# Kernel optimization log

Measured on AMD Instinct MI355X. Metric: run time of the kernel, lower is better.

The kernel has to match this reference:

```python
import jax, jax.numpy as jnp
import numpy as np

WS = 7           # window_size
DIM_HEAD = 32    # qk head dim
NUM_HEAD = 8     # dim_in // dim_head = 256 // 32
DIM_EXP = 1024   # dim_in * exp_ratio
WIN_NUM = 16     # (28 // 7) ** 2
EPS = 1e-5


def _rel_pos_index():
    # same construction as torch buffer; returns [49*49] int index into (2*WS-1)^2 table
    coords = np.stack(np.meshgrid(np.arange(WS), np.arange(WS), indexing='ij'))  # [2,WS,WS]
    cf = coords.reshape(2, -1)                                                   # [2,49]
    rel = cf[:, :, None] - cf[:, None, :]                                        # [2,49,49]
    rel = rel.transpose(1, 2, 0)
    rel[:, :, 0] += WS - 1
    rel[:, :, 1] += WS - 1
    rel[:, :, 0] *= 2 * WS - 1
    return jnp.asarray(rel.sum(-1).reshape(-1), dtype=jnp.int32)                 # [2401]


def _ln_channel(x, w, b):
    # LayerNorm over channel dim (axis=1) of [b,c,h,w], per the 'ln_1d' norm
    mu = jnp.mean(x, axis=1, keepdims=True)
    var = jnp.var(x, axis=1, keepdims=True)
    xn = (x - mu) * jax.lax.rsqrt(var + EPS)
    return xn * w[None, :, None, None] + b[None, :, None, None]


def setup_inputs() -> dict:
    key = jax.random.key(0)
    ks = jax.random.split(key, 12)
    C = 256
    x = jax.random.normal(ks[0], (64, C, 28, 28), dtype=jnp.float32)
    return {
        'x': x,
        'pre_w': jnp.ones((C,), jnp.float32),
        'pre_b': jnp.zeros((C,), jnp.float32),
        'qk_w': jax.random.normal(ks[1], (2 * C, C), jnp.float32) * 0.02,
        'qk_b': jnp.zeros((2 * C,), jnp.float32),
        'v_w': jax.random.normal(ks[2], (DIM_EXP, C), jnp.float32) * 0.02,
        'v_b': jnp.zeros((DIM_EXP,), jnp.float32),
        'post_w': jnp.ones((DIM_EXP // 2,), jnp.float32),
        'post_b': jnp.zeros((DIM_EXP // 2,), jnp.float32),
        'proj_w': jax.random.normal(ks[3], (C, DIM_EXP), jnp.float32) * 0.02,
        'proj_b': jnp.zeros((C,), jnp.float32),
        'rpb_table': jax.random.normal(ks[4], (WIN_NUM, (2 * WS - 1) ** 2, NUM_HEAD), jnp.float32) * 0.02,
    }


def reference(x, pre_w, pre_b, qk_w, qk_b, v_w, v_b, post_w, post_b, proj_w, proj_b, rpb_table):
    B, C, H, W = x.shape
    n1, n2 = H // WS, W // WS
    shortcut = x
    # b c (h1 n1) (w1 n2) -> (b n1 n2) c h1 w1
    xw = x.reshape(B, C, WS, n1, WS, n2).transpose(0, 3, 5, 1, 2, 4).reshape(B * n1 * n2, C, WS, WS)
    b = B * n1 * n2
    xw = _ln_channel(xw, pre_w, pre_b)
    # 1x1 conv QK -> split into q,k per head: channels ordered (qk, heads, dim_head)
    qk = jnp.einsum('oc,bchw->bohw', qk_w, xw) + qk_b[None, :, None, None]
    qk = qk.reshape(b, 2, NUM_HEAD, DIM_HEAD, WS * WS).transpose(1, 0, 2, 4, 3)  # [2,b,h,49,dh]
    q, k = qk[0], qk[1]
    # 1x1 conv V -> attn half + idle half
    v = jnp.einsum('oc,bchw->bohw', v_w, xw) + v_b[None, :, None, None]
    v_attn, v_idle = jnp.split(v, 2, axis=1)                                     # each [b,512,7,7]
    dhv = (DIM_EXP // 2) // NUM_HEAD
    va = v_attn.reshape(b, NUM_HEAD, dhv, WS * WS).transpose(0, 1, 3, 2)         # [b,h,49,dhv]
    # relative position bias (gathered fresh each forward, one table per window)
    idx = _rel_pos_index()
    bias = rpb_table[:, idx, :]                                                  # [wn,2401,nh]
    bias = bias.reshape(WIN_NUM, WS * WS, WS * WS, NUM_HEAD).transpose(0, 3, 1, 2)
    bias = jnp.broadcast_to(bias[None], (B, WIN_NUM, NUM_HEAD, WS * WS, WS * WS)).reshape(b, NUM_HEAD, WS * WS, WS * WS)
    # SDPA (scale = 1/sqrt(q head dim), additive float mask)
    scale = DIM_HEAD ** -0.5
    logits = jnp.einsum('bhqd,bhkd->bhqk', q, k) * scale + bias
    attn = jax.nn.softmax(logits, axis=-1)
    out = jnp.einsum('bhqk,bhkd->bhqd', attn, va)                                # [b,h,49,dhv]
    out = out.transpose(0, 1, 3, 2).reshape(b, DIM_EXP // 2, WS, WS)
    out = _ln_channel(out, post_w, post_b)
    xc = jnp.concatenate([out, v_idle], axis=1)                                  # [b,dim_exp,7,7]
    # (b n1 n2) c h1 w1 -> b c (h1 n1) (w1 n2)
    xc = xc.reshape(B, n1, n2, DIM_EXP, WS, WS).transpose(0, 3, 4, 1, 5, 2).reshape(B, DIM_EXP, H, W)
    xc = jax.nn.gelu(xc, approximate=False)
    xc = jnp.einsum('oc,bchw->bohw', proj_w, xc) + proj_b[None, :, None, None]
    y = shortcut + xc
    return jnp.roll(y, shift=(2, 2), axis=(2, 3))
```

## Files before the change

### kernel.cpp

```cpp
#include <hip/hip_runtime.h>
#include <hip/hip_bf16.h>

typedef __bf16          bf16x8 __attribute__((ext_vector_type(8)));
typedef float           f32x4  __attribute__((ext_vector_type(4)));
typedef unsigned int    u32x2  __attribute__((ext_vector_type(2)));
typedef unsigned int    u32x4v __attribute__((ext_vector_type(4)));

#define QKW_OFF  0
#define VW_OFF   262144
#define PJW_OFF  786432
#define BIAS_OFF 1310720
#define TEMP_OFF 3407872
#define XT_OFF   70516736

#define MFMA(a,b,c) __builtin_amdgcn_mfma_f32_16x16x32_bf16((a),(b),(c),0,0,0)
#define ZERO4 ((f32x4){0.f,0.f,0.f,0.f})
#define CBAR() asm volatile("" ::: "memory")

#define SXN_AT(row, byte)      ((((row)*512 + (byte))) ^ ((((row)&7))<<4))
#define RGB(j)                 (25088 + (j)*6400)
#define RG_AT(base, row, byte) (((base) + (row)*128 + (byte)) ^ (((row)&7)<<4))
#define SC_AT(row, byte)       ((25088 + (row)*512 + (byte)) ^ (((row)&7)<<4))
#define TP_AT(row, byte)       ((((row)*256 + (byte))) ^ (((row)&15)<<4))

static __device__ __forceinline__ unsigned cvtpk(float lo, float hi){
  unsigned r;
  asm("v_cvt_pk_bf16_f32 %0, %1, %2" : "=v"(r) : "v"(lo), "v"(hi));
  return r;
}
static __device__ __forceinline__ unsigned short f2bu(float f) {
  unsigned u = __builtin_bit_cast(unsigned, f);
  return (unsigned short)((u + 0x7FFFu + ((u >> 16) & 1u)) >> 16);
}
static __device__ __forceinline__ float gelu_f(float v){
  return v / (1.f + __expf(-1.5957691216057308f*v*(1.f + 0.044715f*v*v)));
}

__global__ void emo_prep_w(const float* __restrict__ qk_w, const float* __restrict__ v_w,
                           const float* __restrict__ proj_w, unsigned short* __restrict__ w16) {
  int i = blockIdx.x * 256 + threadIdx.x;
  if (i >= 655360) return;
  float v;
  if (i < 131072)      v = qk_w[i];
  else if (i < 393216) v = v_w[i - 131072];
  else                 v = proj_w[i - 393216];
  unsigned u = __builtin_bit_cast(unsigned, v);
  w16[i] = (unsigned short)((u + 0x7FFFu + ((u >> 16) & 1u)) >> 16);
}

__global__ void emo_prep_bias(const float* __restrict__ rpb, float* __restrict__ bx) {
  const int wh = blockIdx.x;
  const int win = wh >> 3, h = wh & 7;
  for (int e = threadIdx.x; e < 4096; e += 256) {
    const int chunk = e >> 8, lane = (e >> 2) & 63, r = e & 3;
    const int mt = chunk >> 2, nt = chunk & 3;
    const int m = mt*16 + (lane >> 4)*4 + r;
    const int n = nt*16 + (lane & 15);
    float v;
    if (n >= 49)      v = -1e30f;
    else if (m >= 49) v = 0.f;
    else {
      const int dI = m/7 - n/7 + 6;
      const int dJ = m%7 - n%7 + 6;
      v = rpb[(win*169 + dI*13 + dJ)*8 + h];
    }
    bx[wh*4096 + e] = v;
  }
}

__global__ __launch_bounds__(256)
void emo_prep_x(const float* __restrict__ x, const float* __restrict__ pre_w,
                const float* __restrict__ pre_b, unsigned short* __restrict__ xt) {
  __shared__ float lv[32*257];
  __shared__ float ps1[8][32];
  __shared__ float ps2[8][32];
  const int tid = threadIdx.x, lane = tid & 63, wv = tid >> 6;
  const int l32 = lane & 31, hp = lane >> 5;
  const int chunk = blockIdx.x, b = blockIdx.y;
  const int s = chunk*32 + l32;
  const bool ok = s < 784;
  const float* xb = x + (size_t)b*200704;
  float s1 = 0.f, s2 = 0.f;
  const int c0 = wv*64 + hp*32;
  for (int ci = 0; ci < 32; ++ci) {
    const int c = c0 + ci;
    const float v = ok ? xb[c*784 + s] : 0.f;
    lv[l32*257 + c] = v;
    s1 += v; s2 += v*v;
  }
  ps1[wv*2 + hp][l32] = s1;
  ps2[wv*2 + hp][l32] = s2;
  __syncthreads();
  const int px = tid & 31, j = tid >> 5;
  const int sp = chunk*32 + px;
  if (sp < 784) {
    float t1 = 0.f, t2 = 0.f;
    #pragma unroll
    for (int k = 0; k < 8; ++k) { t1 += ps1[k][px]; t2 += ps2[k][px]; }
    const float mu = t1*(1.f/256.f);
    const float rs = rsqrtf(t2*(1.f/256.f) - mu*mu + 1e-5f);
    const int h = sp/28, w = sp - h*28;
    const int win = (h & 3)*4 + (w & 3);
    const int wpx = (h >> 2)*7 + (w >> 2);
    unsigned short* row = xt + (((size_t)b*16 + win)*49 + wpx)*256 + j*32;
    #pragma unroll
    for (int g = 0; g < 4; ++g) {
      float gg[8];
      #pragma unroll
      for (int i2 = 0; i2 < 8; ++i2) {
        const int c = j*32 + g*8 + i2;
        gg[i2] = (lv[px*257 + c] - mu)*rs*pre_w[c] + pre_b[c];
      }
      u32x4v pk = { cvtpk(gg[0],gg[1]), cvtpk(gg[2],gg[3]), cvtpk(gg[4],gg[5]), cvtpk(gg[6],gg[7]) };
      *(u32x4v*)(row + g*8) = pk;
    }
  }
}

__global__ __launch_bounds__(512, 4)
void emo_main(const float* __restrict__ qk_b,  const float* __restrict__ v_b,
              const float* __restrict__ post_w,const float* __restrict__ post_b,
              const char*  __restrict__ wsc,
              float* __restrict__ temp)
{
  extern __shared__ char smem[];
  const int tid  = threadIdx.x;
  const int lane = tid & 63;
  const int l16  = lane & 15;
  const int lk   = lane >> 4;
  const int wv   = tid >> 6;
  const int bid  = blockIdx.x;
  const int Bi   = (bid >> 3) & 63;
  const int win  = ((bid & 7) << 1) | (bid >> 9);
  const int SCR  = RGB(wv);

  {
    const unsigned short* xw = (const unsigned short*)(wsc + XT_OFF)
                             + ((size_t)Bi*16 + win)*(49*256);
    for (int p = wv; p < 49; p += 8) {
      const u32x2 d = *(const u32x2*)(xw + p*256 + lane*4);
      *(u32x2*)(smem + SXN_AT(p, lane*8)) = d;
    }
  }
  __syncthreads();

  f32x4 aq[2][4], ak[2][4];
  #pragma unroll
  for (int mt = 0; mt < 2; ++mt)
    #pragma unroll
    for (int nt = 0; nt < 4; ++nt) { aq[mt][nt] = ZERO4; ak[mt][nt] = ZERO4; }
  #pragma unroll 2
  for (int kt = 0; kt < 8; ++kt) {
    bf16x8 bx[4];
    #pragma unroll
    for (int nt = 0; nt < 4; ++nt) {
      const int row = nt*16 + l16, rc = row < 49 ? row : 48;
      bx[nt] = *(const bf16x8*)(smem + SXN_AT(rc, kt*64 + lk*16));
    }
    #pragma unroll
    for (int mt = 0; mt < 2; ++mt) {
      const bf16x8 awq = *(const bf16x8*)(wsc + QKW_OFF + (size_t)(      wv*32 + mt*16 + l16)*512 + kt*64 + lk*16);
      const bf16x8 awk = *(const bf16x8*)(wsc + QKW_OFF + (size_t)(256 + wv*32 + mt*16 + l16)*512 + kt*64 + lk*16);
      #pragma unroll
      for (int nt = 0; nt < 4; ++nt) {
        aq[mt][nt] = MFMA(awq, bx[nt], aq[mt][nt]);
        ak[mt][nt] = MFMA(awk, bx[nt], ak[mt][nt]);
      }
    }
  }
  {
    const f32x4 bq0 = *(const f32x4*)(qk_b +       wv*32 +      lk*4);
    const f32x4 bq1 = *(const f32x4*)(qk_b +       wv*32 + 16 + lk*4);
    const f32x4 bk0 = *(const f32x4*)(qk_b + 256 + wv*32 +      lk*4);
    const f32x4 bk1 = *(const f32x4*)(qk_b + 256 + wv*32 + 16 + lk*4);
    #pragma unroll
    for (int nt = 0; nt < 4; ++nt) {
      aq[0][nt] += bq0; aq[1][nt] += bq1; ak[0][nt] += bk0; ak[1][nt] += bk1;
    }
  }

  #pragma unroll
  for (int nt = 0; nt < 4; ++nt) {
    const int px = nt*16 + l16;
    if (px < 49) {
      #pragma unroll
      for (int mt = 0; mt < 2; ++mt) {
        u32x2 pq  = { cvtpk(aq[mt][nt][0], aq[mt][nt][1]), cvtpk(aq[mt][nt][2], aq[mt][nt][3]) };
        u32x2 pk2 = { cvtpk(ak[mt][nt][0], ak[mt][nt][1]), cvtpk(ak[mt][nt][2], ak[mt][nt][3]) };
        *(u32x2*)(smem + RG_AT(SCR, px,      (mt*16 + lk*4)*2)) = pq;
        *(u32x2*)(smem + RG_AT(SCR, px, 64 + (mt*16 + lk*4)*2)) = pk2;
      }
    }
  }
  CBAR();

  bf16x8 qa[4], kb[4];
  #pragma unroll
  for (int t = 0; t < 4; ++t) {
    const int row = t*16 + l16, rc = row < 49 ? row : 48;
    qa[t] = *(const bf16x8*)(smem + RG_AT(SCR, rc,      lk*16));
    kb[t] = *(const bf16x8*)(smem + RG_AT(SCR, rc, 64 + lk*16));
  }

  f32x4 s[4][4];
  {
    const float scale = 0.17677669529663689f;
    const float* bxp = (const float*)(wsc + BIAS_OFF) + (size_t)(win*8 + wv)*4096 + lane*4;
    #pragma unroll
    for (int mt = 0; mt < 4; ++mt)
      #pragma unroll
      for (int nt = 0; nt < 4; ++nt) {
        f32x4 z = MFMA(qa[mt], kb[nt], ZERO4);
        s[mt][nt] = z*scale + *(const f32x4*)(bxp + (mt*4 + nt)*256);
      }
  }
  #pragma unroll
  for (int mt = 0; mt < 4; ++mt) {
    #pragma unroll
    for (int r = 0; r < 4; ++r) {
      float mx = fmaxf(fmaxf(s[mt][0][r], s[mt][1][r]), fmaxf(s[mt][2][r], s[mt][3][r]));
      mx = fmaxf(mx, __shfl_xor(mx, 1)); mx = fmaxf(mx, __shfl_xor(mx, 2));
      mx = fmaxf(mx, __shfl_xor(mx, 4)); mx = fmaxf(mx, __shfl_xor(mx, 8));
      const float e0 = __expf(s[mt][0][r]-mx), e1 = __expf(s[mt][1][r]-mx);
      const float e2 = __expf(s[mt][2][r]-mx), e3 = __expf(s[mt][3][r]-mx);
      float sm = e0+e1+e2+e3;
      sm += __shfl_xor(sm, 1); sm += __shfl_xor(sm, 2);
      sm += __shfl_xor(sm, 4); sm += __shfl_xor(sm, 8);
      const float inv = 1.f/sm;
      s[mt][0][r] = e0*inv; s[mt][1][r] = e1*inv;
      s[mt][2][r] = e2*inv; s[mt][3][r] = e3*inv;
    }
  }
  #pragma unroll
  for (int mt = 0; mt < 4; ++mt)
    #pragma unroll
    for (int r = 0; r < 4; ++r) {
      const int q = mt*16 + lk*4 + r;
      if (q < 49) {
        #pragma unroll
        for (int nt = 0; nt < 4; ++nt)
          *(unsigned short*)(smem + RG_AT(SCR, q, (nt*16 + l16)*2)) = f2bu(s[mt][nt][r]);
      }
    }
  CBAR();

  f32x4 av[4][4];
  #pragma unroll
  for (int mt = 0; mt < 4; ++mt)
    #pragma unroll
    for (int nt = 0; nt < 4; ++nt) av[mt][nt] = ZERO4;
  #pragma unroll 2
  for (int kt = 0; kt < 8; ++kt) {
    bf16x8 ax[4], bw[4];
    #pragma unroll
    for (int t = 0; t < 4; ++t) {
      const int row = t*16 + l16, rc = row < 49 ? row : 48;
      ax[t] = *(const bf16x8*)(smem + SXN_AT(rc, kt*64 + lk*16));
      bw[t] = *(const bf16x8*)(wsc + VW_OFF + (size_t)(wv*64 + t*16 + l16)*512 + kt*64 + lk*16);
    }
    #pragma unroll
    for (int mt = 0; mt < 4; ++mt)
      #pragma unroll
      for (int nt = 0; nt < 4; ++nt) av[mt][nt] = MFMA(ax[mt], bw[nt], av[mt][nt]);
  }
  {
    #pragma unroll
    for (int nt = 0; nt < 4; ++nt) {
      const float vb = v_b[wv*64 + nt*16 + l16];
      #pragma unroll
      for (int mt = 0; mt < 4; ++mt)
        #pragma unroll
        for (int r = 0; r < 4; ++r) av[mt][nt][r] += vb;
    }
  }

  bf16x8 fpb[4][2];
  #pragma unroll
  for (int t = 0; t < 4; ++t) {
    const int row = t*16 + l16, rc = row < 49 ? row : 48;
    #pragma unroll
    for (int kt = 0; kt < 2; ++kt)
      fpb[t][kt] = *(const bf16x8*)(smem + RG_AT(SCR, rc, (kt*32 + lk*8)*2));
  }
  CBAR();

  f32x4 o[4][4];
  #pragma unroll
  for (int h2 = 0; h2 < 2; ++h2) {
    #pragma unroll
    for (int tc = 0; tc < 2; ++tc) {
      const int nt = h2*2 + tc;
      const int chrow = tc*16 + l16;
      #pragma unroll
      for (int mt = 0; mt < 4; ++mt) {
        u32x2 pv = { cvtpk(av[mt][nt][0], av[mt][nt][1]), cvtpk(av[mt][nt][2], av[mt][nt][3]) };
        *(u32x2*)(smem + RG_AT(SCR, chrow, (mt*16 + lk*4)*2)) = pv;
      }
    }
    CBAR();
    #pragma unroll
    for (int tc = 0; tc < 2; ++tc) {
      const int mtc = h2*2 + tc;
      const bf16x8 a0 = *(const bf16x8*)(smem + RG_AT(SCR, tc*16 + l16, (     lk*8)*2));
      const bf16x8 a1 = *(const bf16x8*)(smem + RG_AT(SCR, tc*16 + l16, (32 + lk*8)*2));
      #pragma unroll
      for (int nt = 0; nt < 4; ++nt) {
        f32x4 z = MFMA(a0, fpb[nt][0], ZERO4);
        o[mtc][nt] = MFMA(a1, fpb[nt][1], z);
      }
    }
    CBAR();
  }

  #pragma unroll
  for (int mtc = 0; mtc < 4; ++mtc)
    #pragma unroll
    for (int nt = 0; nt < 4; ++nt) {
      const int q = nt*16 + l16;
      if (q < 49) {
        u32x2 pk = { cvtpk(o[mtc][nt][0], o[mtc][nt][1]), cvtpk(o[mtc][nt][2], o[mtc][nt][3]) };
        *(u32x2*)(smem + RG_AT(RGB(wv), q, (mtc*16 + lk*4)*2)) = pk;
      }
    }
  __syncthreads();

  {
    const int px = tid >> 3, j = tid & 7;
    if (px < 49) {
      bf16x8 f[8];
      float s1 = 0.f, s2 = 0.f;
      #pragma unroll
      for (int c8 = 0; c8 < 8; ++c8) {
        f[c8] = *(const bf16x8*)(smem + RG_AT(RGB(j), px, c8*16));
        #pragma unroll
        for (int i = 0; i < 8; ++i) { const float v = (float)f[c8][i]; s1 += v; s2 += v*v; }
      }
      s1 += __shfl_xor(s1, 1); s1 += __shfl_xor(s1, 2); s1 += __shfl_xor(s1, 4);
      s2 += __shfl_xor(s2, 1); s2 += __shfl_xor(s2, 2); s2 += __shfl_xor(s2, 4);
      const float mu = s1*(1.f/512.f);
      const float rs = rsqrtf(s2*(1.f/512.f) - mu*mu + 1e-5f);
      #pragma unroll
      for (int c8 = 0; c8 < 8; ++c8) {
        const f32x4 pw0 = *(const f32x4*)(post_w + j*64 + c8*8);
        const f32x4 pw1 = *(const f32x4*)(post_w + j*64 + c8*8 + 4);
        const f32x4 pb0 = *(const f32x4*)(post_b + j*64 + c8*8);
        const f32x4 pb1 = *(const f32x4*)(post_b + j*64 + c8*8 + 4);
        float g[8];
        #pragma unroll
        for (int i = 0; i < 8; ++i) {
          const float v = (float)f[c8][i];
          const float w = i < 4 ? pw0[i] : pw1[i-4];
          const float b = i < 4 ? pb0[i] : pb1[i-4];
          g[i] = gelu_f((v-mu)*rs*w + b);
        }
        u32x4v pk = { cvtpk(g[0],g[1]), cvtpk(g[2],g[3]), cvtpk(g[4],g[5]), cvtpk(g[6],g[7]) };
        *(u32x4v*)(smem + RG_AT(RGB(j), px, c8*16)) = pk;
      }
    }
  }
  __syncthreads();

  f32x4 pacc[2][4];
  #pragma unroll
  for (int mt = 0; mt < 2; ++mt)
    #pragma unroll
    for (int nt = 0; nt < 4; ++nt) pacc[mt][nt] = ZERO4;
  for (int j8 = 0; j8 < 8; ++j8) {
    #pragma unroll
    for (int kt2 = 0; kt2 < 2; ++kt2) {
      bf16x8 b[4];
      #pragma unroll
      for (int nt = 0; nt < 4; ++nt) {
        const int row = nt*16 + l16, rc = row < 49 ? row : 48;
        b[nt] = *(const bf16x8*)(smem + RG_AT(RGB(j8), rc, (kt2*32 + lk*8)*2));
      }
      const int kg = j8*64 + kt2*32 + lk*8;
      #pragma unroll
      for (int mt = 0; mt < 2; ++mt) {
        const bf16x8 aw = *(const bf16x8*)(wsc + PJW_OFF + (size_t)(wv*32 + mt*16 + l16)*2048 + kg*2);
        #pragma unroll
        for (int nt = 0; nt < 4; ++nt) pacc[mt][nt] = MFMA(aw, b[nt], pacc[mt][nt]);
      }
    }
  }
  for (int half = 0; half < 2; ++half) {
    __syncthreads();
    f32x4 ia[2][4];
    #pragma unroll
    for (int mt = 0; mt < 2; ++mt)
      #pragma unroll
      for (int nt = 0; nt < 4; ++nt) ia[mt][nt] = ZERO4;
    const int r0 = 512 + half*256 + wv*32;
    #pragma unroll 2
    for (int kt = 0; kt < 8; ++kt) {
      bf16x8 b[4];
      #pragma unroll
      for (int nt = 0; nt < 4; ++nt) {
        const int row = nt*16 + l16, rc = row < 49 ? row : 48;
        b[nt] = *(const bf16x8*)(smem + SXN_AT(rc, kt*64 + lk*16));
      }
      #pragma unroll
      for (int mt = 0; mt < 2; ++mt) {
        const bf16x8 aw = *(const bf16x8*)(wsc + VW_OFF + (size_t)(r0 + mt*16 + l16)*512 + kt*64 + lk*16);
        #pragma unroll
        for (int nt = 0; nt < 4; ++nt) ia[mt][nt] = MFMA(aw, b[nt], ia[mt][nt]);
      }
    }
    #pragma unroll
    for (int mt = 0; mt < 2; ++mt) {
      const f32x4 vb = *(const f32x4*)(v_b + r0 + mt*16 + lk*4);
      #pragma unroll
      for (int nt = 0; nt < 4; ++nt) {
        const int px = nt*16 + l16;
        const int chl = wv*32 + mt*16 + lk*4;
        u32x2 pk = { cvtpk(gelu_f(ia[mt][nt][0]+vb[0]), gelu_f(ia[mt][nt][1]+vb[1])),
                     cvtpk(gelu_f(ia[mt][nt][2]+vb[2]), gelu_f(ia[mt][nt][3]+vb[3])) };
        *(u32x2*)(smem + SC_AT(px, chl*2)) = pk;
      }
    }
    __syncthreads();
    #pragma unroll 2
    for (int kt = 0; kt < 8; ++kt) {
      bf16x8 b[4];
      #pragma unroll
      for (int nt = 0; nt < 4; ++nt) {
        const int row = nt*16 + l16;
        b[nt] = *(const bf16x8*)(smem + SC_AT(row, (kt*32 + lk*8)*2));
      }
      const int kg = 512 + half*256 + kt*32 + lk*8;
      #pragma unroll
      for (int mt = 0; mt < 2; ++mt) {
        const bf16x8 aw = *(const bf16x8*)(wsc + PJW_OFF + (size_t)(wv*32 + mt*16 + l16)*2048 + kg*2);
        #pragma unroll
        for (int nt = 0; nt < 4; ++nt) pacc[mt][nt] = MFMA(aw, b[nt], pacc[mt][nt]);
      }
    }
  }

  __syncthreads();
  {
    #pragma unroll
    for (int mt = 0; mt < 2; ++mt)
      #pragma unroll
      for (int r = 0; r < 4; ++r) {
        const int row = wv*32 + mt*16 + lk*4 + r;
        #pragma unroll
        for (int nt = 0; nt < 4; ++nt)
          *(float*)(smem + TP_AT(row, (nt*16 + l16)*4)) = pacc[mt][nt][r];
      }
    CBAR();
    float* tb = temp + ((size_t)Bi*16 + win)*(256*64);
    #pragma unroll
    for (int rep = 0; rep < 8; ++rep) {
      const int idx = rep*64 + lane;
      const int row = wv*32 + (idx >> 4);
      const int ch  = idx & 15;
      *(f32x4*)(tb + row*64 + ch*4) = *(const f32x4*)(smem + TP_AT(row, ch*16));
    }
  }
}

__global__ __launch_bounds__(512)
void emo_epi(const float* __restrict__ x, const float* __restrict__ temp,
             const float* __restrict__ proj_b, float* __restrict__ out) {
  extern __shared__ float lv[];
  const int b  = blockIdx.x >> 4;
  const int ct = blockIdx.x & 15;
  const int tid = threadIdx.x, lane = tid & 63, wv = tid >> 6;
  const float* tbb = temp + (size_t)b*262144;
  for (int rr = wv; rr < 256; rr += 8) {
    const int win = rr >> 4, cc = rr & 15;
    const float v = tbb[(size_t)(win*256 + ct*16 + cc)*64 + lane];
    if (lane < 49) {
      const int ph = lane / 7, pw = lane - ph*7;
      const int h = ph*4 + (win >> 2), w = pw*4 + (win & 3);
      lv[cc*812 + h*29 + w] = v;
    }
  }
  __syncthreads();
  const float* xb = x + (size_t)b*200704;
  float* ob       = out + (size_t)b*200704;
  for (int cc = 0; cc < 16; ++cc) {
    const int c = ct*16 + cc;
    const float pb = proj_b[c];
    for (int i = tid; i < 784; i += 512) {
      const int h = i / 28, w = i - h*28;
      int hs = h - 2; if (hs < 0) hs += 28;
      int ws2 = w - 2; if (ws2 < 0) ws2 += 28;
      ob[c*784 + i] = xb[c*784 + hs*28 + ws2] + lv[cc*812 + hs*29 + ws2] + pb;
    }
  }
}

extern "C" void kernel_launch(void* const* d_in, const int* in_sizes, int n_in,
                              void* d_out, int out_size, void* d_ws, size_t ws_size,
                              hipStream_t stream) {
  const float* x      = (const float*)d_in[0];
  const float* pre_w  = (const float*)d_in[1];
  const float* pre_b  = (const float*)d_in[2];
  const float* qk_w   = (const float*)d_in[3];
  const float* qk_b   = (const float*)d_in[4];
  const float* v_w    = (const float*)d_in[5];
  const float* v_b    = (const float*)d_in[6];
  const float* post_w = (const float*)d_in[7];
  const float* post_b = (const float*)d_in[8];
  const float* proj_w = (const float*)d_in[9];
  const float* proj_b = (const float*)d_in[10];
  const float* rpb    = (const float*)d_in[11];
  float* outp = (float*)d_out;
  char* wsc = (char*)d_ws;

  hipFuncSetAttribute((const void*)emo_main, hipFuncAttributeMaxDynamicSharedMemorySize, 81920);
  hipFuncSetAttribute((const void*)emo_epi,  hipFuncAttributeMaxDynamicSharedMemorySize, 53248);

  emo_prep_w<<<2560, 256, 0, stream>>>(qk_w, v_w, proj_w, (unsigned short*)wsc);
  emo_prep_bias<<<128, 256, 0, stream>>>(rpb, (float*)(wsc + BIAS_OFF));
  emo_prep_x<<<dim3(25, 64), 256, 0, stream>>>(x, pre_w, pre_b,
                                               (unsigned short*)(wsc + XT_OFF));
  emo_main<<<1024, 512, 76288, stream>>>(qk_b, v_b, post_w, post_b,
                                         (const char*)wsc, (float*)(wsc + TEMP_OFF));
  emo_epi<<<1024, 512, 51968, stream>>>(x, (const float*)(wsc + TEMP_OFF), proj_b, outp);
}
```

Baseline: 325.7 us.

## Raise MFMA wave priority, fully unroll GEMM loops, merge weight and bias prep kernels

Wraps each MFMA burst in s_setprio(1)/s_setprio(0) so waves issuing matrix ops get scheduling priority over waves doing loads. Changes several K loops from unroll 2 to full unroll so the compiler can schedule loads further ahead. Merges the weight-conversion and bias-expansion prep kernels into one launch to remove a kernel launch. Full unrolling raises register pressure and code size, which could reduce occupancy.

Result: slower. 409.4 us (+25.7%).

```diff
diff --git a/kernel.cpp b/kernel.cpp
--- a/kernel.cpp
+++ b/kernel.cpp
@@ -16,6 +16,7 @@
 #define MFMA(a,b,c) __builtin_amdgcn_mfma_f32_16x16x32_bf16((a),(b),(c),0,0,0)
 #define ZERO4 ((f32x4){0.f,0.f,0.f,0.f})
 #define CBAR() asm volatile("" ::: "memory")
+#define PRIO(n) __builtin_amdgcn_s_setprio(n)
 
 #define SXN_AT(row, byte)      ((((row)*512 + (byte))) ^ ((((row)&7))<<4))
 #define RGB(j)                 (25088 + (j)*6400)
@@ -36,35 +37,37 @@
   return v / (1.f + __expf(-1.5957691216057308f*v*(1.f + 0.044715f*v*v)));
 }
 
-__global__ void emo_prep_w(const float* __restrict__ qk_w, const float* __restrict__ v_w,
-                           const float* __restrict__ proj_w, unsigned short* __restrict__ w16) {
-  int i = blockIdx.x * 256 + threadIdx.x;
-  if (i >= 655360) return;
-  float v;
-  if (i < 131072)      v = qk_w[i];
-  else if (i < 393216) v = v_w[i - 131072];
-  else                 v = proj_w[i - 393216];
-  unsigned u = __builtin_bit_cast(unsigned, v);
-  w16[i] = (unsigned short)((u + 0x7FFFu + ((u >> 16) & 1u)) >> 16);
-}
-
-__global__ void emo_prep_bias(const float* __restrict__ rpb, float* __restrict__ bx) {
-  const int wh = blockIdx.x;
-  const int win = wh >> 3, h = wh & 7;
-  for (int e = threadIdx.x; e < 4096; e += 256) {
-    const int chunk = e >> 8, lane = (e >> 2) & 63, r = e & 3;
-    const int mt = chunk >> 2, nt = chunk & 3;
-    const int m = mt*16 + (lane >> 4)*4 + r;
-    const int n = nt*16 + (lane & 15);
+__global__ void emo_prep_wb(const float* __restrict__ qk_w, const float* __restrict__ v_w,
+                            const float* __restrict__ proj_w, const float* __restrict__ rpb,
+                            unsigned short* __restrict__ w16, float* __restrict__ bx) {
+  const int blk = blockIdx.x;
+  if (blk < 2560) {
+    int i = blk * 256 + threadIdx.x;
+    if (i >= 655360) return;
     float v;
-    if (n >= 49)      v = -1e30f;
-    else if (m >= 49) v = 0.f;
-    else {
-      const int dI = m/7 - n/7 + 6;
-      const int dJ = m%7 - n%7 + 6;
-      v = rpb[(win*169 + dI*13 + dJ)*8 + h];
-    }
-    bx[wh*4096 + e] = v;
+    if (i < 131072)      v = qk_w[i];
+    else if (i < 393216) v = v_w[i - 131072];
+    else                 v = proj_w[i - 393216];
+    unsigned u = __builtin_bit_cast(unsigned, v);
+    w16[i] = (unsigned short)((u + 0x7FFFu + ((u >> 16) & 1u)) >> 16);
+  } else {
+    const int wh = blk - 2560;
+    const int win = wh >> 3, h = wh & 7;
+    for (int e = threadIdx.x; e < 4096; e += 256) {
+      const int chunk = e >> 8, lane = (e >> 2) & 63, r = e & 3;
+      const int mt = chunk >> 2, nt = chunk & 3;
+      const int m = mt*16 + (lane >> 4)*4 + r;
+      const int n = nt*16 + (lane & 15);
+      float v;
+      if (n >= 49)      v = -1e30f;
+      else if (m >= 49) v = 0.f;
+      else {
+        const int dI = m/7 - n/7 + 6;
+        const int dJ = m%7 - n%7 + 6;
+        v = rpb[(win*169 + dI*13 + dJ)*8 + h];
+      }
+      bx[wh*4096 + e] = v;
+    }
   }
 }
 
@@ -149,7 +152,7 @@
   for (int mt = 0; mt < 2; ++mt)
     #pragma unroll
     for (int nt = 0; nt < 4; ++nt) { aq[mt][nt] = ZERO4; ak[mt][nt] = ZERO4; }
-  #pragma unroll 2
+  #pragma unroll
   for (int kt = 0; kt < 8; ++kt) {
     bf16x8 bx[4];
     #pragma unroll
@@ -161,11 +164,13 @@
     for (int mt = 0; mt < 2; ++mt) {
       const bf16x8 awq = *(const bf16x8*)(wsc + QKW_OFF + (size_t)(      wv*32 + mt*16 + l16)*512 + kt*64 + lk*16);
       const bf16x8 awk = *(const bf16x8*)(wsc + QKW_OFF + (size_t)(256 + wv*32 + mt*16 + l16)*512 + kt*64 + lk*16);
+      PRIO(1);
       #pragma unroll
       for (int nt = 0; nt < 4; ++nt) {
         aq[mt][nt] = MFMA(awq, bx[nt], aq[mt][nt]);
         ak[mt][nt] = MFMA(awk, bx[nt], ak[mt][nt]);
       }
+      PRIO(0);
     }
   }
   {
@@ -206,6 +211,7 @@
   {
     const float scale = 0.17677669529663689f;
     const float* bxp = (const float*)(wsc + BIAS_OFF) + (size_t)(win*8 + wv)*4096 + lane*4;
+    PRIO(1);
     #pragma unroll
     for (int mt = 0; mt < 4; ++mt)
       #pragma unroll
@@ -213,6 +219,7 @@
         f32x4 z = MFMA(qa[mt], kb[nt], ZERO4);
         s[mt][nt] = z*scale + *(const f32x4*)(bxp + (mt*4 + nt)*256);
       }
+    PRIO(0);
   }
   #pragma unroll
   for (int mt = 0; mt < 4; ++mt) {
@@ -249,7 +256,7 @@
   for (int mt = 0; mt < 4; ++mt)
     #pragma unroll
     for (int nt = 0; nt < 4; ++nt) av[mt][nt] = ZERO4;
-  #pragma unroll 2
+  #pragma unroll
   for (int kt = 0; kt < 8; ++kt) {
     bf16x8 ax[4], bw[4];
     #pragma unroll
@@ -258,10 +265,12 @@
       ax[t] = *(const bf16x8*)(smem + SXN_AT(rc, kt*64 + lk*16));
       bw[t] = *(const bf16x8*)(wsc + VW_OFF + (size_t)(wv*64 + t*16 + l16)*512 + kt*64 + lk*16);
     }
+    PRIO(1);
     #pragma unroll
     for (int mt = 0; mt < 4; ++mt)
       #pragma unroll
       for (int nt = 0; nt < 4; ++nt) av[mt][nt] = MFMA(ax[mt], bw[nt], av[mt][nt]);
+    PRIO(0);
   }
   {
     #pragma unroll
@@ -303,11 +312,13 @@
       const int mtc = h2*2 + tc;
       const bf16x8 a0 = *(const bf16x8*)(smem + RG_AT(SCR, tc*16 + l16, (     lk*8)*2));
       const bf16x8 a1 = *(const bf16x8*)(smem + RG_AT(SCR, tc*16 + l16, (32 + lk*8)*2));
+      PRIO(1);
       #pragma unroll
       for (int nt = 0; nt < 4; ++nt) {
         f32x4 z = MFMA(a0, fpb[nt][0], ZERO4);
         o[mtc][nt] = MFMA(a1, fpb[nt][1], z);
       }
+      PRIO(0);
     }
     CBAR();
   }
@@ -365,6 +376,7 @@
   for (int mt = 0; mt < 2; ++mt)
     #pragma unroll
     for (int nt = 0; nt < 4; ++nt) pacc[mt][nt] = ZERO4;
+  #pragma unroll
   for (int j8 = 0; j8 < 8; ++j8) {
     #pragma unroll
     for (int kt2 = 0; kt2 < 2; ++kt2) {
@@ -378,11 +390,14 @@
       #pragma unroll
       for (int mt = 0; mt < 2; ++mt) {
         const bf16x8 aw = *(const bf16x8*)(wsc + PJW_OFF + (size_t)(wv*32 + mt*16 + l16)*2048 + kg*2);
+        PRIO(1);
         #pragma unroll
         for (int nt = 0; nt < 4; ++nt) pacc[mt][nt] = MFMA(aw, b[nt], pacc[mt][nt]);
-      }
-    }
-  }
+        PRIO(0);
+      }
+    }
+  }
+  #pragma unroll 1
   for (int half = 0; half < 2; ++half) {
     __syncthreads();
     f32x4 ia[2][4];
@@ -391,7 +406,7 @@
       #pragma unroll
       for (int nt = 0; nt < 4; ++nt) ia[mt][nt] = ZERO4;
     const int r0 = 512 + half*256 + wv*32;
-    #pragma unroll 2
+    #pragma unroll
     for (int kt = 0; kt < 8; ++kt) {
       bf16x8 b[4];
       #pragma unroll
@@ -402,8 +417,10 @@
       #pragma unroll
       for (int mt = 0; mt < 2; ++mt) {
         const bf16x8 aw = *(const bf16x8*)(wsc + VW_OFF + (size_t)(r0 + mt*16 + l16)*512 + kt*64 + lk*16);
+        PRIO(1);
         #pragma unroll
         for (int nt = 0; nt < 4; ++nt) ia[mt][nt] = MFMA(aw, b[nt], ia[mt][nt]);
+        PRIO(0);
       }
     }
     #pragma unroll
@@ -419,7 +436,7 @@
       }
     }
     __syncthreads();
-    #pragma unroll 2
+    #pragma unroll
     for (int kt = 0; kt < 8; ++kt) {
       bf16x8 b[4];
       #pragma unroll
@@ -431,8 +448,10 @@
       #pragma unroll
       for (int mt = 0; mt < 2; ++mt) {
         const bf16x8 aw = *(const bf16x8*)(wsc + PJW_OFF + (size_t)(wv*32 + mt*16 + l16)*2048 + kg*2);
+        PRIO(1);
         #pragma unroll
         for (int nt = 0; nt < 4; ++nt) pacc[mt][nt] = MFMA(aw, b[nt], pacc[mt][nt]);
+        PRIO(0);
       }
     }
   }
@@ -513,8 +532,8 @@
   hipFuncSetAttribute((const void*)emo_main, hipFuncAttributeMaxDynamicSharedMemorySize, 81920);
   hipFuncSetAttribute((const void*)emo_epi,  hipFuncAttributeMaxDynamicSharedMemorySize, 53248);
 
-  emo_prep_w<<<2560, 256, 0, stream>>>(qk_w, v_w, proj_w, (unsigned short*)wsc);
-  emo_prep_bias<<<128, 256, 0, stream>>>(rpb, (float*)(wsc + BIAS_OFF));
+  emo_prep_wb<<<2688, 256, 0, stream>>>(qk_w, v_w, proj_w, rpb,
+                                        (unsigned short*)wsc, (float*)(wsc + BIAS_OFF));
   emo_prep_x<<<dim3(25, 64), 256, 0, stream>>>(x, pre_w, pre_b,
                                                (unsigned short*)(wsc + XT_OFF));
   emo_main<<<1024, 512, 76288, stream>>>(qk_b, v_b, post_w, post_b,
```
